# Performance work log

Hardware: AMD Instinct MI355X
Metric: run time of the kernel (lower is better)

Reference implementation:

```python
import jax, jax.numpy as jnp
import numpy as np

WEIGHT_HARD = 0.5
WEIGHT_SOFT = 0.5
BETA = 0.5
IGNORE_INDEX = -100
TEMPERATURE = 1.0

N_TOK = 2048
H_STU = 2048
H_TEA = 4096
VOCAB = 32000


def setup_inputs() -> dict:
    key = jax.random.key(0)
    k1, k2, k3, k4, k5 = jax.random.split(key, 5)
    scale_s = 1.0 / np.sqrt(H_STU)
    scale_t = 1.0 / np.sqrt(H_TEA)
    return {
        "student_input": jax.random.normal(k1, (N_TOK, H_STU), dtype=jnp.float32),
        "student_weight": jax.random.normal(k2, (VOCAB, H_STU), dtype=jnp.float32) * scale_s,
        "teacher_input": jax.random.normal(k3, (N_TOK, H_TEA), dtype=jnp.float32),
        "teacher_weight": jax.random.normal(k4, (VOCAB, H_TEA), dtype=jnp.float32) * scale_t,
        "true_labels": jax.random.randint(k5, (N_TOK,), 0, VOCAB, dtype=jnp.int64),
    }


def reference(student_input, student_weight, teacher_input, teacher_weight, true_labels):
    n = student_input.shape[0]
    # Fused linear projections: (BT, H) @ (H, V) -> (BT, V)
    s_logits = jnp.einsum("nh,vh->nv", student_input, student_weight).astype(jnp.float32)
    t_logits = jnp.einsum("nh,vh->nv", teacher_input, teacher_weight).astype(jnp.float32)

    # Hard loss: NLL on un-tempered student log-probs, sum over valid, / total N
    s_lp = jax.nn.log_softmax(s_logits, axis=-1)
    valid = true_labels != IGNORE_INDEX
    safe_labels = jnp.where(valid, true_labels, 0)
    picked = jnp.take_along_axis(s_lp, safe_labels[:, None], axis=1)[:, 0]
    hard_loss = jnp.sum(jnp.where(valid, -picked, 0.0)) / n

    # Soft loss: generalized JSD on temperature-scaled logits, sum over all tokens, / N
    s_lp_t = jax.nn.log_softmax(s_logits / TEMPERATURE, axis=-1)
    t_lp_t = jax.nn.log_softmax(t_logits / TEMPERATURE, axis=-1)
    s_p = jnp.exp(s_lp_t)
    t_p = jnp.exp(t_lp_t)
    log_mean = jnp.log(BETA * s_p + (1.0 - BETA) * t_p)
    student_kl = jnp.sum(s_p * (s_lp_t - log_mean))  # KL(student || mean)
    teacher_kl = jnp.sum(t_p * (t_lp_t - log_mean))  # KL(teacher || mean)
    jsd = BETA * teacher_kl + (1.0 - BETA) * student_kl
    soft_loss = jsd / n

    return WEIGHT_HARD * hard_loss + WEIGHT_SOFT * soft_loss
```

## Files before the change

kernel.cpp:

```cpp
#include <hip/hip_runtime.h>
#include <stdint.h>

#define AS1C(p) ((const __attribute__((address_space(1))) void*)(p))
#define AS3(p)  ((__attribute__((address_space(3))) void*)(p))

typedef short bf16x8 __attribute__((ext_vector_type(8)));
typedef float f32x4  __attribute__((ext_vector_type(4)));
typedef unsigned short u16x8 __attribute__((ext_vector_type(8)));

static __device__ __forceinline__ unsigned pack_bf16_2(float lo, float hi) {
  return (__float_as_uint(lo) >> 16) | (__float_as_uint(hi) & 0xFFFF0000u);
}
static __device__ __forceinline__ unsigned short bf16_rnd(float v) {
  return (unsigned short)((__float_as_uint(v) + 0x8000u) >> 16);
}
static __device__ __forceinline__ float bf16_f(unsigned short u) {
  return __uint_as_float(((unsigned)u) << 16);
}

__global__ __launch_bounds__(256) void cvt_f32_bf16(const float* __restrict__ in,
                                                    uint2* __restrict__ out,
                                                    long long n4) {
  long long i = (long long)blockIdx.x * blockDim.x + threadIdx.x;
  long long stride = (long long)gridDim.x * blockDim.x;
  const float4* in4 = (const float4*)in;
  for (; i < n4; i += stride) {
    float4 v = in4[i];
    uint2 o;
    o.x = pack_bf16_2(v.x, v.y);
    o.y = pack_bf16_2(v.z, v.w);
    out[i] = o;
  }
}


static __device__ __forceinline__ void stage2(const short* __restrict__ G, int K,
                                              int grow0, int k0,
                                              short* lds, int tid) {
  const int rl = tid >> 3;
  const int ks = ((tid & 7) ^ (rl & 7)) << 3;
  const short* src = G + (size_t)(grow0 + rl) * K + k0 + ks;
  short* dst = lds + (tid >> 6) * 512;
  __builtin_amdgcn_global_load_lds(AS1C(src), AS3(dst), 16, 0, 0);
  __builtin_amdgcn_global_load_lds(AS1C(src + (size_t)64 * K), AS3(dst + 4096), 16, 0, 0);
}

#define MFMA16(IM0, JN0)                                                        \
  __builtin_amdgcn_s_setprio(1);                                                \
  _Pragma("unroll")                                                             \
  for (int mi = 0; mi < 4; ++mi) {                                              \
    _Pragma("unroll")                                                           \
    for (int nj = 0; nj < 2; ++nj) {                                            \
      acc[(IM0) + mi][(JN0) + nj] = __builtin_amdgcn_mfma_f32_16x16x32_bf16(    \
          a_[mi][0], b_[(JN0) + nj][0], acc[(IM0) + mi][(JN0) + nj], 0, 0, 0);  \
      acc[(IM0) + mi][(JN0) + nj] = __builtin_amdgcn_mfma_f32_16x16x32_bf16(    \
          a_[mi][1], b_[(JN0) + nj][1], acc[(IM0) + mi][(JN0) + nj], 0, 0, 0);  \
    }                                                                           \
  }                                                                             \
  __builtin_amdgcn_s_setprio(0);

__global__ __launch_bounds__(512, 2) void gemm8p(const short* __restrict__ A,
                                                 const short* __restrict__ B,
                                                 unsigned short* __restrict__ C,
                                                 int N, int K, int mshift, int NT) {
  __shared__ __align__(16) short sA[4 * 8192];
  __shared__ __align__(16) short sB[4 * 8192];

  const int tid = threadIdx.x;
  const int lane = tid & 63;
  const int wv = tid >> 6;
  const int wm = wv >> 2;
  const int wn = wv & 3;

  const int nwg = gridDim.x;
  const int orig = blockIdx.x;
  const int q = nwg >> 3, r = nwg & 7;
  const int xcd = orig & 7;
  const int wg = (xcd < r ? xcd * (q + 1) : r * (q + 1) + (xcd - r) * q) + (orig >> 3);
  const int bm = wg & ((1 << mshift) - 1);
  const int bn = wg >> mshift;

  const int mrow0 = bm << 8;
  const int nrow0 = bn << 8;

  const int lr = lane & 15;
  const int koff0 = (((lane >> 4) << 3) ^ ((lane & 7) << 3));
  const int koff1 = ((32 + ((lane >> 4) << 3)) ^ ((lane & 7) << 3));

  f32x4 acc[8][4] = {};
  bf16x8 a_[4][2], b_[4][2];

  stage2(A, K, mrow0,       0, sA + 0 * 8192, tid);
  stage2(A, K, mrow0 + 128, 0, sA + 1 * 8192, tid);
  stage2(B, K, nrow0,       0, sB + 0 * 8192, tid);
  stage2(B, K, nrow0 + 128, 0, sB + 1 * 8192, tid);
  if (NT > 1) {
    stage2(B, K, nrow0,       64, sB + 2 * 8192, tid);
    stage2(B, K, nrow0 + 128, 64, sB + 3 * 8192, tid);
    asm volatile("s_waitcnt vmcnt(4)" ::: "memory");
  } else {
    asm volatile("s_waitcnt vmcnt(0)" ::: "memory");
  }
  __builtin_amdgcn_s_barrier();

  for (int t = 0; t < NT; ++t) {
    const int P = t & 1;
    const short* aB = sA + (P * 2 + wm) * 8192;
    const short* bB = sB + (P * 2 + (wn >> 1)) * 8192;
    const int bcol = (wn & 1) * 64;

    #pragma unroll
    for (int mi = 0; mi < 4; ++mi) {
      a_[mi][0] = *(const bf16x8*)&aB[(mi * 16 + lr) * 64 + koff0];
      a_[mi][1] = *(const bf16x8*)&aB[(mi * 16 + lr) * 64 + koff1];
    }
    #pragma unroll
    for (int nj = 0; nj < 2; ++nj) {
      const int cb = (bcol + nj * 16 + lr) * 64;
      b_[nj][0] = *(const bf16x8*)&bB[cb + koff0];
      b_[nj][1] = *(const bf16x8*)&bB[cb + koff1];
    }
    if (t + 1 < NT) stage2(A, K, mrow0, (t + 1) * 64, sA + ((P ^ 1) * 2) * 8192, tid);
    __builtin_amdgcn_s_barrier();
    MFMA16(0, 0)
    __builtin_amdgcn_s_barrier();

    #pragma unroll
    for (int nj = 0; nj < 2; ++nj) {
      const int cb = (bcol + (nj + 2) * 16 + lr) * 64;
      b_[nj + 2][0] = *(const bf16x8*)&bB[cb + koff0];
      b_[nj + 2][1] = *(const bf16x8*)&bB[cb + koff1];
    }
    if (t + 1 < NT) stage2(A, K, mrow0 + 128, (t + 1) * 64, sA + ((P ^ 1) * 2 + 1) * 8192, tid);
    __builtin_amdgcn_s_barrier();
    MFMA16(0, 2)
    __builtin_amdgcn_s_barrier();

    #pragma unroll
    for (int mi = 0; mi < 4; ++mi) {
      a_[mi][0] = *(const bf16x8*)&aB[(64 + mi * 16 + lr) * 64 + koff0];
      a_[mi][1] = *(const bf16x8*)&aB[(64 + mi * 16 + lr) * 64 + koff1];
    }
    if (t + 2 < NT) stage2(B, K, nrow0, (t + 2) * 64, sB + (P * 2) * 8192, tid);
    __builtin_amdgcn_s_barrier();
    MFMA16(4, 2)
    __builtin_amdgcn_s_barrier();

    if (t + 2 < NT) stage2(B, K, nrow0 + 128, (t + 2) * 64, sB + (P * 2 + 1) * 8192, tid);
    __builtin_amdgcn_s_barrier();
    MFMA16(4, 0)
    if (t + 2 < NT) asm volatile("s_waitcnt vmcnt(4)" ::: "memory");
    else            asm volatile("s_waitcnt vmcnt(0)" ::: "memory");
    __builtin_amdgcn_s_barrier();
  }

  #pragma unroll
  for (int im = 0; im < 8; ++im) {
    const int row = mrow0 + wm * 128 + im * 16 + ((lane >> 4) << 2);
    #pragma unroll
    for (int ni = 0; ni < 4; ++ni) {
      const int col = nrow0 + wn * 64 + ni * 16 + lr;
      #pragma unroll
      for (int rr = 0; rr < 4; ++rr)
        C[(size_t)(row + rr) * N + col] = bf16_rnd(acc[im][ni][rr]);
    }
  }
}

__global__ __launch_bounds__(256) void gemm_lean(const float* __restrict__ A,
                                                 const float* __restrict__ B,
                                                 unsigned short* __restrict__ C,
                                                 int N, int K) {
  __shared__ __align__(16) short sA[128 * 64];
  __shared__ __align__(16) short sB[128 * 64];
  const int t = threadIdx.x;
  const int lane = t & 63;
  const int wv = t >> 6;
  const int wm = wv >> 1, wn = wv & 1;
  const int rowA0 = blockIdx.x * 128;
  const int rowB0 = blockIdx.y * 128;

  f32x4 acc[4][4] = {};

  for (int k0 = 0; k0 < K; k0 += 64) {
    #pragma unroll
    for (int i = 0; i < 8; ++i) {
      const int o = i * 1024 + t * 4;
      const int row = o >> 6;
      const int kcol = o & 63;
      const int dst = row * 64 + (kcol ^ ((row & 7) << 3));
      float4 va = *(const float4*)(A + (size_t)(rowA0 + row) * K + k0 + kcol);
      float4 vb = *(const float4*)(B + (size_t)(rowB0 + row) * K + k0 + kcol);
      uint2 pa, pb;
      pa.x = pack_bf16_2(va.x, va.y); pa.y = pack_bf16_2(va.z, va.w);
      pb.x = pack_bf16_2(vb.x, vb.y); pb.y = pack_bf16_2(vb.z, vb.w);
      *(uint2*)(sA + dst) = pa;
      *(uint2*)(sB + dst) = pb;
    }
    __syncthreads();
    #pragma unroll
    for (int kk = 0; kk < 2; ++kk) {
      bf16x8 af[4], bfr[4];
      #pragma unroll
      for (int mi = 0; mi < 4; ++mi) {
        const int row = wm * 64 + mi * 16 + (lane & 15);
        const int koff = (kk * 32 + (lane >> 4) * 8) ^ ((row & 7) << 3);
        af[mi] = *(const bf16x8*)&sA[row * 64 + koff];
      }
      #pragma unroll
      for (int ni = 0; ni < 4; ++ni) {
        const int col = wn * 64 + ni * 16 + (lane & 15);
        const int koff = (kk * 32 + (lane >> 4) * 8) ^ ((col & 7) << 3);
        bfr[ni] = *(const bf16x8*)&sB[col * 64 + koff];
      }
      #pragma unroll
      for (int mi = 0; mi < 4; ++mi)
        #pragma unroll
        for (int ni = 0; ni < 4; ++ni)
          acc[mi][ni] = __builtin_amdgcn_mfma_f32_16x16x32_bf16(af[mi], bfr[ni],
                                                                acc[mi][ni], 0, 0, 0);
    }
    __syncthreads();
  }

  #pragma unroll
  for (int mi = 0; mi < 4; ++mi)
    #pragma unroll
    for (int ni = 0; ni < 4; ++ni) {
      const int col = rowB0 + wn * 64 + ni * 16 + (lane & 15);
      const int rowb = rowA0 + wm * 64 + mi * 16 + ((lane >> 4) * 4);
      #pragma unroll
      for (int r = 0; r < 4; ++r)
        C[(size_t)(rowb + r) * N + col] = bf16_rnd(acc[mi][ni][r]);
    }
}

__global__ __launch_bounds__(512) void fused_loss(const unsigned short* __restrict__ SL,
                                                  const unsigned short* __restrict__ TL,
                                                  int V,
                                                  const int* __restrict__ labels,
                                                  int rowOff, float* __restrict__ acc) {
  __shared__ __align__(16) unsigned short bufS[32768];
  __shared__ __align__(16) unsigned short bufT[32768];
  __shared__ float red[4][8];
  const int row = blockIdx.x;
  const int tid = threadIdx.x;
  const u16x8* ps = (const u16x8*)(SL + (size_t)row * V);
  const u16x8* pt = (const u16x8*)(TL + (size_t)row * V);
  const int n8 = V >> 3;

  float ms = -1e30f, ss = 0.f, mt = -1e30f, st = 0.f;
  for (int i = tid; i < n8; i += 512) {
    u16x8 a = ps[i], b = pt[i];
    *(u16x8*)&bufS[i * 8] = a;
    *(u16x8*)&bufT[i * 8] = b;
    float lmS = -1e30f, lmT = -1e30f;
    float fa[8], fb[8];
    #pragma unroll
    for (int j = 0; j < 8; ++j) {
      fa[j] = bf16_f(a[j]); fb[j] = bf16_f(b[j]);
      lmS = fmaxf(lmS, fa[j]); lmT = fmaxf(lmT, fb[j]);
    }
    if (lmS > ms) { ss *= __expf(ms - lmS); ms = lmS; }
    if (lmT > mt) { st *= __expf(mt - lmT); mt = lmT; }
    #pragma unroll
    for (int j = 0; j < 8; ++j) {
      ss += __expf(fa[j] - ms);
      st += __expf(fb[j] - mt);
    }
  }
  #pragma unroll
  for (int off = 32; off > 0; off >>= 1) {
    float mo = __shfl_xor(ms, off), so = __shfl_xor(ss, off);
    float mn = fmaxf(ms, mo);
    ss = ss * __expf(ms - mn) + so * __expf(mo - mn); ms = mn;
    mo = __shfl_xor(mt, off); so = __shfl_xor(st, off);
    mn = fmaxf(mt, mo);
    st = st * __expf(mt - mn) + so * __expf(mo - mn); mt = mn;
  }
  const int w = tid >> 6;
  if ((tid & 63) == 0) { red[0][w] = ms; red[1][w] = ss; red[2][w] = mt; red[3][w] = st; }
  __syncthreads();
  __shared__ float lse2[2];
  if (tid == 0) {
    float M = red[0][0], S = red[1][0];
    for (int i = 1; i < 8; ++i) {
      float mn = fmaxf(M, red[0][i]);
      S = S * __expf(M - mn) + red[1][i] * __expf(red[0][i] - mn); M = mn;
    }
    lse2[0] = M + __logf(S);
    M = red[2][0]; S = red[3][0];
    for (int i = 1; i < 8; ++i) {
      float mn = fmaxf(M, red[2][i]);
      S = S * __expf(M - mn) + red[3][i] * __expf(red[2][i] - mn); M = mn;
    }
    lse2[1] = M + __logf(S);
  }
  __syncthreads();
  const float slse = lse2[0], tlse = lse2[1];
  const int lbl = labels[rowOff + row];

  float jsd = 0.f, hard = 0.f;
  for (int i = tid; i < n8; i += 512) {
    u16x8 a = *(const u16x8*)&bufS[i * 8];
    u16x8 b = *(const u16x8*)&bufT[i * 8];
    #pragma unroll
    for (int j = 0; j < 8; ++j) {
      float sl = bf16_f(a[j]) - slse;
      float tl = bf16_f(b[j]) - tlse;
      float sp = __expf(sl), tp = __expf(tl);
      float lm = __logf(0.5f * (sp + tp));
      jsd += 0.5f * (tp * (tl - lm) + sp * (sl - lm));
      if (i * 8 + j == lbl) hard = -sl;
    }
  }
  #pragma unroll
  for (int off = 32; off > 0; off >>= 1) {
    jsd += __shfl_xor(jsd, off);
    hard += __shfl_xor(hard, off);
  }
  if ((tid & 63) == 0) { red[0][w] = jsd; red[1][w] = hard; }
  __syncthreads();
  if (tid == 0) {
    float J = 0.f, H = 0.f;
    for (int i = 0; i < 8; ++i) { J += red[0][i]; H += red[1][i]; }
    atomicAdd(&acc[0], H);
    atomicAdd(&acc[1], J);
  }
}

__global__ void finalize_loss(const float* __restrict__ acc, float* __restrict__ out,
                              float invn) {
  out[0] = 0.5f * acc[0] * invn + 0.5f * acc[1] * invn;
}

extern "C" void kernel_launch(void* const* d_in, const int* in_sizes, int n_in,
                              void* d_out, int out_size, void* d_ws, size_t ws_size,
                              hipStream_t stream) {
  const float* sIn = (const float*)d_in[0];
  const float* sW  = (const float*)d_in[1];
  const float* tIn = (const float*)d_in[2];
  const float* tW  = (const float*)d_in[3];
  const int*   lbl = (const int*)d_in[4];

  const int N  = in_sizes[4];
  const int HS = in_sizes[0] / N;
  const int HT = in_sizes[2] / N;
  const int V  = in_sizes[1] / HS;

  char* ws = (char*)d_ws;
  size_t off = 0;
  auto alloc = [&](size_t b) { size_t p = off; off = (off + b + 255) & ~(size_t)255; return p; };

  const size_t o_sInB = alloc((size_t)N * HS * 2);
  const size_t o_tInB = alloc((size_t)N * HT * 2);
  const size_t o_acc  = alloc(256);

  const bool shapeOK = (V % 256 == 0) && (V <= 32768) && (V % 8 == 0) &&
                       (HS % 64 == 0) && (HT % 64 == 0) && (N % 256 == 0);
  const size_t weightBytes = (size_t)V * HS * 2 + (size_t)V * HT * 2 + 512;
  const size_t minLogits   = 2ull * 256 * V * 2 + 512;
  const bool full = shapeOK && (off + weightBytes + minLogits) <= ws_size;
  size_t o_sWB = 0, o_tWB = 0;
  if (full) {
    o_sWB = alloc((size_t)V * HS * 2);
    o_tWB = alloc((size_t)V * HT * 2);
  }

  size_t avail = ws_size > off ? ws_size - off : 0;
  int Rfit = (int)(avail / (2ull * V * 2));
  int R = full ? 256 : 128;
  while (R * 2 <= Rfit && R * 2 <= N) R *= 2;
  const size_t o_sL = alloc((size_t)R * V * 2);
  const size_t o_tL = alloc((size_t)R * V * 2);

  hipMemsetAsync(ws + o_acc, 0, 8, stream);

  if (full) {
    auto cvt = [&](const float* src, size_t dstOff, size_t n) {
      long long n4 = (long long)(n / 4);
      int grid = (int)((n4 + 255) / 256);
      if (grid > 2048) grid = 2048;
      cvt_f32_bf16<<<grid, 256, 0, stream>>>(src, (uint2*)(ws + dstOff), n4);
    };
    cvt(sIn, o_sInB, (size_t)N * HS);
    cvt(tIn, o_tInB, (size_t)N * HT);
    cvt(sW,  o_sWB,  (size_t)V * HS);
    cvt(tW,  o_tWB,  (size_t)V * HT);
  }

  const int Mt = R / 256;
  int mshift = 0;
  while ((1 << mshift) < Mt) ++mshift;

  for (int r0 = 0; r0 < N; r0 += R) {
    if (full) {
      gemm8p<<<Mt * (V / 256), 512, 0, stream>>>(
          (const short*)(ws + o_sInB + (size_t)r0 * HS * 2), (const short*)(ws + o_sWB),
          (unsigned short*)(ws + o_sL), V, HS, mshift, HS / 64);
      gemm8p<<<Mt * (V / 256), 512, 0, stream>>>(
          (const short*)(ws + o_tInB + (size_t)r0 * HT * 2), (const short*)(ws + o_tWB),
          (unsigned short*)(ws + o_tL), V, HT, mshift, HT / 64);
    } else {
      dim3 g(R / 128, V / 128);
      gemm_lean<<<g, 256, 0, stream>>>(sIn + (size_t)r0 * HS, sW,
                                       (unsigned short*)(ws + o_sL), V, HS);
      gemm_lean<<<g, 256, 0, stream>>>(tIn + (size_t)r0 * HT, tW,
                                       (unsigned short*)(ws + o_tL), V, HT);
    }
    fused_loss<<<R, 512, 0, stream>>>((const unsigned short*)(ws + o_sL),
                                      (const unsigned short*)(ws + o_tL), V,
                                      lbl, r0, (float*)(ws + o_acc));
  }

  finalize_loss<<<1, 1, 0, stream>>>((float*)(ws + o_acc), (float*)d_out, 1.0f / N);
}
```

Baseline: 1.155 ms.

## Fuse fp32-to-bf16 weight conversion into GEMM B-tile loading

```diff
diff --git a/kernel.cpp b/kernel.cpp
--- a/kernel.cpp
+++ b/kernel.cpp
@@ -43,6 +43,30 @@
   short* dst = lds + (tid >> 6) * 512;
   __builtin_amdgcn_global_load_lds(AS1C(src), AS3(dst), 16, 0, 0);
   __builtin_amdgcn_global_load_lds(AS1C(src + (size_t)64 * K), AS3(dst + 4096), 16, 0, 0);
+}
+
+static __device__ __forceinline__ void loadB(const float* __restrict__ B, int K,
+                                             int grow0, int k0, int tid, float4* r) {
+  const int row = tid >> 2;
+  const int kb = (tid & 3) << 4;
+  const float* s = B + (size_t)(grow0 + row) * K + k0 + kb;
+  r[0] = *(const float4*)(s);
+  r[1] = *(const float4*)(s + 4);
+  r[2] = *(const float4*)(s + 8);
+  r[3] = *(const float4*)(s + 12);
+}
+
+static __device__ __forceinline__ void writeB(short* buf, int tid, const float4* r) {
+  const int row = tid >> 2;
+  const int g0 = (tid & 3) << 1;
+  uint4 w0, w1;
+  w0.x = pack_bf16_2(r[0].x, r[0].y); w0.y = pack_bf16_2(r[0].z, r[0].w);
+  w0.z = pack_bf16_2(r[1].x, r[1].y); w0.w = pack_bf16_2(r[1].z, r[1].w);
+  w1.x = pack_bf16_2(r[2].x, r[2].y); w1.y = pack_bf16_2(r[2].z, r[2].w);
+  w1.z = pack_bf16_2(r[3].x, r[3].y); w1.w = pack_bf16_2(r[3].z, r[3].w);
+  const int x = (row & 7) << 3;
+  *(uint4*)(buf + row * 64 + ((g0 * 8) ^ x))       = w0;
+  *(uint4*)(buf + row * 64 + (((g0 + 1) * 8) ^ x)) = w1;
 }
 
 #define MFMA16(IM0, JN0)                                                        \
@@ -59,10 +83,10 @@
   }                                                                             \
   __builtin_amdgcn_s_setprio(0);
 
-__global__ __launch_bounds__(512, 2) void gemm8p(const short* __restrict__ A,
-                                                 const short* __restrict__ B,
-                                                 unsigned short* __restrict__ C,
-                                                 int N, int K, int mshift, int NT) {
+__global__ __launch_bounds__(512, 2) void gemm8pf(const short* __restrict__ A,
+                                                  const float* __restrict__ B,
+                                                  unsigned short* __restrict__ C,
+                                                  int N, int K, int mshift, int NT) {
   __shared__ __align__(16) short sA[4 * 8192];
   __shared__ __align__(16) short sB[4 * 8192];
 
@@ -89,17 +113,20 @@
 
   f32x4 acc[8][4] = {};
   bf16x8 a_[4][2], b_[4][2];
+  float4 rB0[4], rB1[4];
 
   stage2(A, K, mrow0,       0, sA + 0 * 8192, tid);
   stage2(A, K, mrow0 + 128, 0, sA + 1 * 8192, tid);
-  stage2(B, K, nrow0,       0, sB + 0 * 8192, tid);
-  stage2(B, K, nrow0 + 128, 0, sB + 1 * 8192, tid);
+  loadB(B, K, nrow0,       0, tid, rB0);
+  loadB(B, K, nrow0 + 128, 0, tid, rB1);
+  writeB(sB + 0 * 8192, tid, rB0);
+  writeB(sB + 1 * 8192, tid, rB1);
   if (NT > 1) {
-    stage2(B, K, nrow0,       64, sB + 2 * 8192, tid);
-    stage2(B, K, nrow0 + 128, 64, sB + 3 * 8192, tid);
-    asm volatile("s_waitcnt vmcnt(4)" ::: "memory");
+    loadB(B, K, nrow0,       64, tid, rB0);
+    loadB(B, K, nrow0 + 128, 64, tid, rB1);
+    asm volatile("s_waitcnt vmcnt(8) lgkmcnt(0)" ::: "memory");
   } else {
-    asm volatile("s_waitcnt vmcnt(0)" ::: "memory");
+    asm volatile("s_waitcnt vmcnt(0) lgkmcnt(0)" ::: "memory");
   }
   __builtin_amdgcn_s_barrier();
 
@@ -107,6 +134,8 @@
     const int P = t & 1;
     const short* aB = sA + (P * 2 + wm) * 8192;
     const short* bB = sB + (P * 2 + (wn >> 1)) * 8192;
+    short* nxA = sA + ((P ^ 1) * 2) * 8192;
+    short* nxB = sB + ((P ^ 1) * 2) * 8192;
     const int bcol = (wn & 1) * 64;
 
     #pragma unroll
@@ -120,7 +149,7 @@
       b_[nj][0] = *(const bf16x8*)&bB[cb + koff0];
       b_[nj][1] = *(const bf16x8*)&bB[cb + koff1];
     }
-    if (t + 1 < NT) stage2(A, K, mrow0, (t + 1) * 64, sA + ((P ^ 1) * 2) * 8192, tid);
+    if (t + 1 < NT) stage2(A, K, mrow0, (t + 1) * 64, nxA, tid);
     __builtin_amdgcn_s_barrier();
     MFMA16(0, 0)
     __builtin_amdgcn_s_barrier();
@@ -131,7 +160,7 @@
       b_[nj + 2][0] = *(const bf16x8*)&bB[cb + koff0];
       b_[nj + 2][1] = *(const bf16x8*)&bB[cb + koff1];
     }
-    if (t + 1 < NT) stage2(A, K, mrow0 + 128, (t + 1) * 64, sA + ((P ^ 1) * 2 + 1) * 8192, tid);
+    if (t + 1 < NT) stage2(A, K, mrow0 + 128, (t + 1) * 64, nxA + 8192, tid);
     __builtin_amdgcn_s_barrier();
     MFMA16(0, 2)
     __builtin_amdgcn_s_barrier();
@@ -141,16 +170,18 @@
       a_[mi][0] = *(const bf16x8*)&aB[(64 + mi * 16 + lr) * 64 + koff0];
       a_[mi][1] = *(const bf16x8*)&aB[(64 + mi * 16 + lr) * 64 + koff1];
     }
-    if (t + 2 < NT) stage2(B, K, nrow0, (t + 2) * 64, sB + (P * 2) * 8192, tid);
+    if (t + 1 < NT) writeB(nxB, tid, rB0);
+    if (t + 2 < NT) loadB(B, K, nrow0, (t + 2) * 64, tid, rB0);
     __builtin_amdgcn_s_barrier();
     MFMA16(4, 2)
     __builtin_amdgcn_s_barrier();
 
-    if (t + 2 < NT) stage2(B, K, nrow0 + 128, (t + 2) * 64, sB + (P * 2 + 1) * 8192, tid);
+    if (t + 1 < NT) writeB(nxB + 8192, tid, rB1);
+    if (t + 2 < NT) loadB(B, K, nrow0 + 128, (t + 2) * 64, tid, rB1);
     __builtin_amdgcn_s_barrier();
     MFMA16(4, 0)
-    if (t + 2 < NT) asm volatile("s_waitcnt vmcnt(4)" ::: "memory");
-    else            asm volatile("s_waitcnt vmcnt(0)" ::: "memory");
+    if (t + 2 < NT) asm volatile("s_waitcnt vmcnt(8) lgkmcnt(0)" ::: "memory");
+    else            asm volatile("s_waitcnt vmcnt(0) lgkmcnt(0)" ::: "memory");
     __builtin_amdgcn_s_barrier();
   }
 
@@ -358,14 +389,8 @@
 
   const bool shapeOK = (V % 256 == 0) && (V <= 32768) && (V % 8 == 0) &&
                        (HS % 64 == 0) && (HT % 64 == 0) && (N % 256 == 0);
-  const size_t weightBytes = (size_t)V * HS * 2 + (size_t)V * HT * 2 + 512;
-  const size_t minLogits   = 2ull * 256 * V * 2 + 512;
-  const bool full = shapeOK && (off + weightBytes + minLogits) <= ws_size;
-  size_t o_sWB = 0, o_tWB = 0;
-  if (full) {
-    o_sWB = alloc((size_t)V * HS * 2);
-    o_tWB = alloc((size_t)V * HT * 2);
-  }
+  const size_t minLogits = 2ull * 256 * V * 2 + 512;
+  const bool full = shapeOK && (off + minLogits) <= ws_size;
 
   size_t avail = ws_size > off ? ws_size - off : 0;
   int Rfit = (int)(avail / (2ull * V * 2));
@@ -385,8 +410,6 @@
     };
     cvt(sIn, o_sInB, (size_t)N * HS);
     cvt(tIn, o_tInB, (size_t)N * HT);
-    cvt(sW,  o_sWB,  (size_t)V * HS);
-    cvt(tW,  o_tWB,  (size_t)V * HT);
   }
 
   const int Mt = R / 256;
@@ -395,11 +418,11 @@
 
   for (int r0 = 0; r0 < N; r0 += R) {
     if (full) {
-      gemm8p<<<Mt * (V / 256), 512, 0, stream>>>(
-          (const short*)(ws + o_sInB + (size_t)r0 * HS * 2), (const short*)(ws + o_sWB),
+      gemm8pf<<<Mt * (V / 256), 512, 0, stream>>>(
+          (const short*)(ws + o_sInB + (size_t)r0 * HS * 2), sW,
           (unsigned short*)(ws + o_sL), V, HS, mshift, HS / 64);
-      gemm8p<<<Mt * (V / 256), 512, 0, stream>>>(
-          (const short*)(ws + o_tInB + (size_t)r0 * HT * 2), (const short*)(ws + o_tWB),
+      gemm8pf<<<Mt * (V / 256), 512, 0, stream>>>(
+          (const short*)(ws + o_tInB + (size_t)r0 * HT * 2), tW,
           (unsigned short*)(ws + o_tL), V, HT, mshift, HT / 64);
     } else {
       dim3 g(R / 128, V / 128);
```

Result: faster. 1.052 ms (-8.9%).
